# Performance work log

Hardware: AMD Instinct MI355X
Metric: run time of the kernel (lower is better)

The kernel has to match this reference:

```python
import jax, jax.numpy as jnp
import numpy as np

EPS = 1e-8  # RMSNormMultiHead default eps (forward passes self.eps)


def rms_norm_multihead(x, weight):
    # x: (B, L, H, d); normalize over last dim in float32, then scale per (H, d)
    x32 = x.astype(jnp.float32)
    normed = x32 * jax.lax.rsqrt(jnp.mean(x32 * x32, axis=-1, keepdims=True) + EPS)
    return normed.astype(x.dtype) * weight


def setup_inputs() -> dict:
    key = jax.random.key(0)
    k0, k1, k2 = jax.random.split(key, 3)
    B, L, D, H = 2, 1024, 1024, 16
    d = D // H
    X = jax.random.normal(k0, (B, L, D), dtype=jnp.float32)
    Wq = jax.random.normal(k1, (D, D), dtype=jnp.float32) * 0.02  # q_proj weight (out, in)
    Wv = jax.random.normal(k2, (D, D), dtype=jnp.float32) * 0.02  # v_proj weight (out, in)
    q_norm_w = jnp.ones((H, d), dtype=jnp.float32)
    v_norm_w = jnp.ones((H, d), dtype=jnp.float32)
    return {"X": X, "Wq": Wq, "Wv": Wv, "q_norm_w": q_norm_w, "v_norm_w": v_norm_w}


def reference(X, Wq, Wv, q_norm_w, v_norm_w):
    B, L, D = X.shape
    H, d = q_norm_w.shape
    K = X.reshape(B, L, H, d)
    Q = rms_norm_multihead((X @ Wq.T).reshape(B, L, H, d), q_norm_w)
    V = rms_norm_multihead((X @ Wv.T).reshape(B, L, H, d), v_norm_w)
    # cumulative outer-product KV state: (B, L, H, d, e)
    W = jnp.cumsum(jnp.einsum('blhd,blhe->blhde', K, V), axis=1)
    out = jnp.einsum('blhd,blhde->blhe', Q, W).reshape(B, L, D)
    return out
```

## Files before the change

### kernel.cpp

```cpp
#include <hip/hip_runtime.h>

#define BB 2
#define LL 1024
#define DD 1024
#define HH 16
#define NC 16
#define EPSF 1e-8f

typedef __attribute__((ext_vector_type(8))) short bf16x8;
typedef __attribute__((ext_vector_type(4))) float f32x4;
typedef unsigned short u16;

static __device__ inline u16 f2bf(float f) {
    unsigned int u = __builtin_bit_cast(unsigned int, f);
    u += 0x7fff + ((u >> 16) & 1);
    return (u16)(u >> 16);
}

static __device__ inline void gload_lds16(const u16* g, u16* l) {
    __builtin_amdgcn_global_load_lds((const __attribute__((address_space(1))) void*)g,
                                     (__attribute__((address_space(3))) void*)l, 16, 0, 0);
}

__global__ __launch_bounds__(256) void cvt_k(const float* __restrict__ X,
                                             const float* __restrict__ Wq,
                                             const float* __restrict__ Wv,
                                             u16* __restrict__ Xb,
                                             u16* __restrict__ Wqb,
                                             u16* __restrict__ Wvb)
{
    int i = (blockIdx.x * 256 + threadIdx.x) * 4;
    const float* s; u16* d; int off;
    if (i < 2*1024*1024)      { s = X;  d = Xb;  off = i; }
    else if (i < 3*1024*1024) { s = Wq; d = Wqb; off = i - 2*1024*1024; }
    else                      { s = Wv; d = Wvb; off = i - 3*1024*1024; }
    float4 v = *(const float4*)(s + off);
    ushort4 o;
    o.x = f2bf(v.x); o.y = f2bf(v.y); o.z = f2bf(v.z); o.w = f2bf(v.w);
    *(ushort4*)(d + off) = o;
}

__global__ __launch_bounds__(256) void gemm_fused(const u16* __restrict__ Xb,
                                                  const u16* __restrict__ Wqb,
                                                  const u16* __restrict__ Wvb,
                                                  const float* __restrict__ qw,
                                                  const float* __restrict__ vw,
                                                  u16* __restrict__ Qb,
                                                  u16* __restrict__ Vb)
{
    const int K = DD, N = DD;
    const u16* W = blockIdx.z ? Wvb : Wqb;
    const float* nw = blockIdx.z ? vw : qw;
    u16* Y = blockIdx.z ? Vb : Qb;
    __shared__ u16 As[128 * 32];
    __shared__ u16 Bs[64 * 32];

    const int tid = threadIdx.x, w = tid >> 6, lane = tid & 63;
    const int quad = lane >> 4, l16 = lane & 15;
    const int m0 = blockIdx.y * 128, n0 = blockIdx.x * 64;
    const int lrow = lane >> 2, lcol = (lane & 3) * 8;

    const u16* gA0 = Xb + (size_t)(m0 + w*16 + lrow) * K + lcol;
    const u16* gA1 = gA0 + (size_t)64 * K;
    const u16* gB0 = W + (size_t)(n0 + w*16 + lrow) * K + lcol;
    u16* lA0 = &As[(w*16) * 32];
    u16* lA1 = &As[(64 + w*16) * 32];
    u16* lB0 = &Bs[(w*16) * 32];

    f32x4 acc[2][4] = {};
    for (int k0 = 0; k0 < K; k0 += 32) {
        gload_lds16(gA0 + k0, lA0);
        gload_lds16(gA1 + k0, lA1);
        gload_lds16(gB0 + k0, lB0);
        __syncthreads();
        bf16x8 af[2], bfr[4];
        #pragma unroll
        for (int i = 0; i < 2; ++i)
            af[i] = *(const bf16x8*)&As[(w*32 + i*16 + l16) * 32 + quad*8];
        #pragma unroll
        for (int j = 0; j < 4; ++j)
            bfr[j] = *(const bf16x8*)&Bs[(j*16 + l16) * 32 + quad*8];
        #pragma unroll
        for (int i = 0; i < 2; ++i)
            #pragma unroll
            for (int j = 0; j < 4; ++j)
                acc[i][j] = __builtin_amdgcn_mfma_f32_16x16x32_bf16(af[i], bfr[j], acc[i][j], 0, 0, 0);
        __syncthreads();
    }

    float wv[4];
    #pragma unroll
    for (int j = 0; j < 4; ++j) wv[j] = nw[n0 + j*16 + l16];
    #pragma unroll
    for (int i = 0; i < 2; ++i) {
        float ss[4];
        #pragma unroll
        for (int r = 0; r < 4; ++r) {
            float s = 0.f;
            #pragma unroll
            for (int j = 0; j < 4; ++j) s += acc[i][j][r] * acc[i][j][r];
            ss[r] = s;
        }
        #pragma unroll
        for (int off = 1; off < 16; off <<= 1)
            #pragma unroll
            for (int r = 0; r < 4; ++r) ss[r] += __shfl_xor(ss[r], off, 64);
        float sc[4];
        #pragma unroll
        for (int r = 0; r < 4; ++r) sc[r] = rsqrtf(ss[r] * (1.f/64.f) + EPSF);
        #pragma unroll
        for (int r = 0; r < 4; ++r) {
            u16* yp = Y + (size_t)(m0 + w*32 + i*16 + quad*4 + r) * N + n0;
            #pragma unroll
            for (int j = 0; j < 4; ++j)
                yp[j*16 + l16] = f2bf(acc[i][j][r] * sc[r] * wv[j]);
        }
    }
}

__global__ __launch_bounds__(256) void kv_scan(const u16* __restrict__ Xb,
                                               const u16* __restrict__ Vb,
                                               u16* __restrict__ S)
{
    const int t = blockIdx.x & 3, bh = blockIdx.x >> 2;
    const int et = t & 1, dt = t >> 1;
    const int h = bh & 15, b = bh >> 4;
    __shared__ u16 Kt[32][72];
    __shared__ u16 Vt[32][72];
    const int tid = threadIdx.x, w = tid >> 6, lane = tid & 63;
    const int quad = lane >> 4, l16 = lane & 15;
    const int esub = (w & 1) * 16, dsub = (w >> 1) * 16;
    const int row = tid >> 2, q = tid & 3;

    const u16* gK = Xb + (size_t)(b*LL + row) * DD + h*64 + dt*32 + q*8;
    const u16* gV = Vb + (size_t)(b*LL + row) * DD + h*64 + et*32 + q*8;

    ushort4 kr[2], vr[2];
    kr[0] = *(const ushort4*)(gK);     kr[1] = *(const ushort4*)(gK + 4);
    vr[0] = *(const ushort4*)(gV);     vr[1] = *(const ushort4*)(gV + 4);

    f32x4 acc = {};
    for (int c = 0; c < NC; ++c) {
        #pragma unroll
        for (int i = 0; i < 4; ++i) {
            Kt[q*8 + i][row]     = ((const u16*)&kr[0])[i];
            Kt[q*8 + 4 + i][row] = ((const u16*)&kr[1])[i];
            Vt[q*8 + i][row]     = ((const u16*)&vr[0])[i];
            Vt[q*8 + 4 + i][row] = ((const u16*)&vr[1])[i];
        }
        __syncthreads();
        if (c + 1 < NC) {
            const u16* nK = gK + (size_t)(c+1)*64*DD;
            const u16* nV = gV + (size_t)(c+1)*64*DD;
            kr[0] = *(const ushort4*)(nK); kr[1] = *(const ushort4*)(nK + 4);
            vr[0] = *(const ushort4*)(nV); vr[1] = *(const ushort4*)(nV + 4);
        }
        u16* Sp = S + ((size_t)bh * NC + c) * 4096;
        #pragma unroll
        for (int r = 0; r < 4; ++r)
            Sp[(et*32 + esub + quad*4 + r) * 64 + dt*32 + dsub + l16] = f2bf(acc[r]);
        #pragma unroll
        for (int k0 = 0; k0 < 64; k0 += 32) {
            bf16x8 av = *(const bf16x8*)&Vt[esub + l16][k0 + quad*8];
            bf16x8 bv = *(const bf16x8*)&Kt[dsub + l16][k0 + quad*8];
            acc = __builtin_amdgcn_mfma_f32_16x16x32_bf16(av, bv, acc, 0, 0, 0);
        }
        __syncthreads();
    }
}

__global__ __launch_bounds__(256) void out_k(const u16* __restrict__ Xb,
                                             const u16* __restrict__ Qb,
                                             const u16* __restrict__ Vb,
                                             const u16* __restrict__ S,
                                             float* __restrict__ out)
{
    const int c = blockIdx.x & 15, bh = blockIdx.x >> 4;
    const int h = bh & 15, b = bh >> 4;
    __shared__ u16 Qs[64][72];
    __shared__ u16 Ks[64][72];
    __shared__ u16 Vt[64][72];
    __shared__ u16 St[64][72];
    const int tid = threadIdx.x;
    {
        const int row = tid >> 2, q = tid & 3;
        size_t gbase = (size_t)(b*LL + c*64 + row) * DD + h*64 + q*16;
        u16 vv[16];
        #pragma unroll
        for (int i = 0; i < 16; i += 4) {
            *(ushort4*)&Qs[row][q*16 + i] = *(const ushort4*)(Qb + gbase + i);
            *(ushort4*)&Ks[row][q*16 + i] = *(const ushort4*)(Xb + gbase + i);
            *(ushort4*)&vv[i] = *(const ushort4*)(Vb + gbase + i);
        }
        #pragma unroll
        for (int i = 0; i < 16; ++i)
            Vt[q*16 + i][row] = vv[i];
        const u16* sp = S + ((size_t)bh * NC + c) * 4096 + row*64 + q*16;
        #pragma unroll
        for (int i = 0; i < 16; i += 4)
            *(ushort4*)&St[row][q*16 + i] = *(const ushort4*)(sp + i);
    }
    __syncthreads();
    const int w = tid >> 6, lane = tid & 63, quad = lane >> 4, l16 = lane & 15;
    const int mo = (w & 1) * 32, no = (w >> 1) * 32;

    f32x4 pacc[2][2] = {};
    #pragma unroll
    for (int k0 = 0; k0 < 64; k0 += 32) {
        bf16x8 aq[2], bk[2];
        #pragma unroll
        for (int i = 0; i < 2; ++i)
            aq[i] = *(const bf16x8*)&Qs[mo + i*16 + l16][k0 + quad*8];
        #pragma unroll
        for (int j = 0; j < 2; ++j)
            bk[j] = *(const bf16x8*)&Ks[no + j*16 + l16][k0 + quad*8];
        #pragma unroll
        for (int i = 0; i < 2; ++i)
            #pragma unroll
            for (int j = 0; j < 2; ++j)
                pacc[i][j] = __builtin_amdgcn_mfma_f32_16x16x32_bf16(aq[i], bk[j], pacc[i][j], 0, 0, 0);
    }
    __syncthreads();
    #pragma unroll
    for (int i = 0; i < 2; ++i)
        #pragma unroll
        for (int j = 0; j < 2; ++j)
            #pragma unroll
            for (int r = 0; r < 4; ++r) {
                int l  = mo + i*16 + quad*4 + r;
                int lp = no + j*16 + l16;
                Ks[l][lp] = (lp <= l) ? f2bf(pacc[i][j][r]) : (u16)0;
            }
    __syncthreads();

    f32x4 acc[2][2] = {};
    #pragma unroll
    for (int k0 = 0; k0 < 64; k0 += 32) {
        bf16x8 a1[2], b1[2], a2[2], b2[2];
        #pragma unroll
        for (int i = 0; i < 2; ++i) {
            a1[i] = *(const bf16x8*)&Ks[mo + i*16 + l16][k0 + quad*8];
            a2[i] = *(const bf16x8*)&Qs[mo + i*16 + l16][k0 + quad*8];
        }
        #pragma unroll
        for (int j = 0; j < 2; ++j) {
            b1[j] = *(const bf16x8*)&Vt[no + j*16 + l16][k0 + quad*8];
            b2[j] = *(const bf16x8*)&St[no + j*16 + l16][k0 + quad*8];
        }
        #pragma unroll
        for (int i = 0; i < 2; ++i)
            #pragma unroll
            for (int j = 0; j < 2; ++j) {
                acc[i][j] = __builtin_amdgcn_mfma_f32_16x16x32_bf16(a1[i], b1[j], acc[i][j], 0, 0, 0);
                acc[i][j] = __builtin_amdgcn_mfma_f32_16x16x32_bf16(a2[i], b2[j], acc[i][j], 0, 0, 0);
            }
    }
    float* op = out + (size_t)(b*LL + c*64) * DD + h*64;
    #pragma unroll
    for (int i = 0; i < 2; ++i)
        #pragma unroll
        for (int j = 0; j < 2; ++j)
            #pragma unroll
            for (int r = 0; r < 4; ++r)
                op[(size_t)(mo + i*16 + quad*4 + r) * DD + no + j*16 + l16] = acc[i][j][r];
}

extern "C" void kernel_launch(void* const* d_in, const int* in_sizes, int n_in,
                              void* d_out, int out_size, void* d_ws, size_t ws_size,
                              hipStream_t stream) {
    const float* X  = (const float*)d_in[0];
    const float* Wq = (const float*)d_in[1];
    const float* Wv = (const float*)d_in[2];
    const float* qw = (const float*)d_in[3];
    const float* vw = (const float*)d_in[4];
    float* out = (float*)d_out;

    u16* Xb  = (u16*)d_ws;
    u16* Wqb = Xb  + (size_t)2*1024*1024;
    u16* Wvb = Wqb + (size_t)1024*1024;
    u16* Qb  = Wvb + (size_t)1024*1024;
    u16* Vb  = Qb  + (size_t)2*1024*1024;
    u16* S   = Vb  + (size_t)2*1024*1024;

    cvt_k<<<4096, 256, 0, stream>>>(X, Wq, Wv, Xb, Wqb, Wvb);
    gemm_fused<<<dim3(16, 16, 2), 256, 0, stream>>>(Xb, Wqb, Wvb, qw, vw, Qb, Vb);
    kv_scan<<<128, 256, 0, stream>>>(Xb, Vb, S);
    out_k<<<BB*HH*NC, 256, 0, stream>>>(Xb, Qb, Vb, S, out);
}
```

Measured before the change: 110.4 us.

## Double-buffer kv_scan, widen GEMM k-step, and coalesce state layout

The projection GEMM now loads two 32-wide K slices per iteration into separate LDS buffers, which halves the number of barrier pairs in the K loop. kv_scan double-buffers its transposed K/V tiles and splits the loading so half the threads fetch K and half fetch V, prefetching two chunks ahead. It also stores the chunk state in MFMA fragment order so writes are contiguous. out_k is updated to decode that permuted layout when filling its LDS tile. The cost is more LDS and registers per block, and a more intricate index mapping between the two kernels.

```diff
diff --git a/kernel.cpp b/kernel.cpp
--- a/kernel.cpp
+++ b/kernel.cpp
@@ -52,8 +52,8 @@
     const u16* W = blockIdx.z ? Wvb : Wqb;
     const float* nw = blockIdx.z ? vw : qw;
     u16* Y = blockIdx.z ? Vb : Qb;
-    __shared__ u16 As[128 * 32];
-    __shared__ u16 Bs[64 * 32];
+    __shared__ u16 As0[128 * 32], As1[128 * 32];
+    __shared__ u16 Bs0[64 * 32],  Bs1[64 * 32];
 
     const int tid = threadIdx.x, w = tid >> 6, lane = tid & 63;
     const int quad = lane >> 4, l16 = lane & 15;
@@ -63,28 +63,36 @@
     const u16* gA0 = Xb + (size_t)(m0 + w*16 + lrow) * K + lcol;
     const u16* gA1 = gA0 + (size_t)64 * K;
     const u16* gB0 = W + (size_t)(n0 + w*16 + lrow) * K + lcol;
-    u16* lA0 = &As[(w*16) * 32];
-    u16* lA1 = &As[(64 + w*16) * 32];
-    u16* lB0 = &Bs[(w*16) * 32];
+    u16* lA0_0 = &As0[(w*16) * 32];      u16* lA0_1 = &As1[(w*16) * 32];
+    u16* lA1_0 = &As0[(64 + w*16) * 32]; u16* lA1_1 = &As1[(64 + w*16) * 32];
+    u16* lB0_0 = &Bs0[(w*16) * 32];      u16* lB0_1 = &Bs1[(w*16) * 32];
 
     f32x4 acc[2][4] = {};
-    for (int k0 = 0; k0 < K; k0 += 32) {
-        gload_lds16(gA0 + k0, lA0);
-        gload_lds16(gA1 + k0, lA1);
-        gload_lds16(gB0 + k0, lB0);
+    for (int k0 = 0; k0 < K; k0 += 64) {
+        gload_lds16(gA0 + k0,      lA0_0);
+        gload_lds16(gA0 + k0 + 32, lA0_1);
+        gload_lds16(gA1 + k0,      lA1_0);
+        gload_lds16(gA1 + k0 + 32, lA1_1);
+        gload_lds16(gB0 + k0,      lB0_0);
+        gload_lds16(gB0 + k0 + 32, lB0_1);
         __syncthreads();
-        bf16x8 af[2], bfr[4];
-        #pragma unroll
-        for (int i = 0; i < 2; ++i)
-            af[i] = *(const bf16x8*)&As[(w*32 + i*16 + l16) * 32 + quad*8];
-        #pragma unroll
-        for (int j = 0; j < 4; ++j)
-            bfr[j] = *(const bf16x8*)&Bs[(j*16 + l16) * 32 + quad*8];
-        #pragma unroll
-        for (int i = 0; i < 2; ++i)
+        #pragma unroll
+        for (int hh = 0; hh < 2; ++hh) {
+            const u16* Ah = hh ? As1 : As0;
+            const u16* Bh = hh ? Bs1 : Bs0;
+            bf16x8 af[2], bfr[4];
+            #pragma unroll
+            for (int i = 0; i < 2; ++i)
+                af[i] = *(const bf16x8*)&Ah[(w*32 + i*16 + l16) * 32 + quad*8];
             #pragma unroll
             for (int j = 0; j < 4; ++j)
-                acc[i][j] = __builtin_amdgcn_mfma_f32_16x16x32_bf16(af[i], bfr[j], acc[i][j], 0, 0, 0);
+                bfr[j] = *(const bf16x8*)&Bh[(j*16 + l16) * 32 + quad*8];
+            #pragma unroll
+            for (int i = 0; i < 2; ++i)
+                #pragma unroll
+                for (int j = 0; j < 4; ++j)
+                    acc[i][j] = __builtin_amdgcn_mfma_f32_16x16x32_bf16(af[i], bfr[j], acc[i][j], 0, 0, 0);
+        }
         __syncthreads();
     }
 
@@ -125,44 +133,42 @@
     const int t = blockIdx.x & 3, bh = blockIdx.x >> 2;
     const int et = t & 1, dt = t >> 1;
     const int h = bh & 15, b = bh >> 4;
-    __shared__ u16 Kt[32][72];
-    __shared__ u16 Vt[32][72];
+    __shared__ u16 Kt[2][32][72];
+    __shared__ u16 Vt[2][32][72];
     const int tid = threadIdx.x, w = tid >> 6, lane = tid & 63;
     const int quad = lane >> 4, l16 = lane & 15;
     const int esub = (w & 1) * 16, dsub = (w >> 1) * 16;
-    const int row = tid >> 2, q = tid & 3;
-
-    const u16* gK = Xb + (size_t)(b*LL + row) * DD + h*64 + dt*32 + q*8;
-    const u16* gV = Vb + (size_t)(b*LL + row) * DD + h*64 + et*32 + q*8;
-
-    ushort4 kr[2], vr[2];
-    kr[0] = *(const ushort4*)(gK);     kr[1] = *(const ushort4*)(gK + 4);
-    vr[0] = *(const ushort4*)(gV);     vr[1] = *(const ushort4*)(gV + 4);
-
+    const int half = tid >> 7, hrow = (tid & 127) >> 1, hq = tid & 1;
+    const u16* gsrc = (half ? Vb : Xb) + (size_t)(b*LL + hrow) * DD
+                      + h*64 + (half ? et : dt) * 32 + hq*16;
+    u16 (*Tb)[32][72] = half ? Vt : Kt;
+    ushort4 rr[4];
+
+    auto loadc = [&](int c) {
+        const u16* p = gsrc + (size_t)c * 64 * DD;
+        rr[0] = *(const ushort4*)(p);      rr[1] = *(const ushort4*)(p + 4);
+        rr[2] = *(const ushort4*)(p + 8);  rr[3] = *(const ushort4*)(p + 12);
+    };
+    auto writec = [&](int buf) {
+        #pragma unroll
+        for (int i = 0; i < 16; ++i)
+            Tb[buf][hq*16 + i][hrow] = ((const u16*)rr)[i];
+    };
+
+    loadc(0); writec(0); loadc(1);
+    __syncthreads();
     f32x4 acc = {};
     for (int c = 0; c < NC; ++c) {
-        #pragma unroll
-        for (int i = 0; i < 4; ++i) {
-            Kt[q*8 + i][row]     = ((const u16*)&kr[0])[i];
-            Kt[q*8 + 4 + i][row] = ((const u16*)&kr[1])[i];
-            Vt[q*8 + i][row]     = ((const u16*)&vr[0])[i];
-            Vt[q*8 + 4 + i][row] = ((const u16*)&vr[1])[i];
-        }
-        __syncthreads();
-        if (c + 1 < NC) {
-            const u16* nK = gK + (size_t)(c+1)*64*DD;
-            const u16* nV = gV + (size_t)(c+1)*64*DD;
-            kr[0] = *(const ushort4*)(nK); kr[1] = *(const ushort4*)(nK + 4);
-            vr[0] = *(const ushort4*)(nV); vr[1] = *(const ushort4*)(nV + 4);
-        }
-        u16* Sp = S + ((size_t)bh * NC + c) * 4096;
-        #pragma unroll
-        for (int r = 0; r < 4; ++r)
-            Sp[(et*32 + esub + quad*4 + r) * 64 + dt*32 + dsub + l16] = f2bf(acc[r]);
+        const int cur = c & 1;
+        if (c + 1 < NC) writec(1 - cur);
+        if (c + 2 < NC) loadc(c + 2);
+        u16* Sp = S + (((size_t)(bh*NC + c)) << 12) + t*1024 + w*256;
+        #pragma unroll
+        for (int r = 0; r < 4; ++r) Sp[r*64 + lane] = f2bf(acc[r]);
         #pragma unroll
         for (int k0 = 0; k0 < 64; k0 += 32) {
-            bf16x8 av = *(const bf16x8*)&Vt[esub + l16][k0 + quad*8];
-            bf16x8 bv = *(const bf16x8*)&Kt[dsub + l16][k0 + quad*8];
+            bf16x8 av = *(const bf16x8*)&Vt[cur][esub + l16][k0 + quad*8];
+            bf16x8 bv = *(const bf16x8*)&Kt[cur][dsub + l16][k0 + quad*8];
             acc = __builtin_amdgcn_mfma_f32_16x16x32_bf16(av, bv, acc, 0, 0, 0);
         }
         __syncthreads();
@@ -195,10 +201,16 @@
         #pragma unroll
         for (int i = 0; i < 16; ++i)
             Vt[q*16 + i][row] = vv[i];
-        const u16* sp = S + ((size_t)bh * NC + c) * 4096 + row*64 + q*16;
-        #pragma unroll
-        for (int i = 0; i < 16; i += 4)
-            *(ushort4*)&St[row][q*16 + i] = *(const ushort4*)(sp + i);
+        const u16* Sc = S + (((size_t)(bh*NC + c)) << 12);
+        #pragma unroll
+        for (int j = 0; j < 4; ++j) {
+            int f = (tid + j*256) * 4;
+            ushort4 sv = *(const ushort4*)(Sc + f);
+            int tt = f >> 10, ww = (f >> 8) & 3, rr_ = (f >> 6) & 3, ln = f & 63;
+            int e = (tt & 1)*32 + (ww & 1)*16 + (ln >> 4)*4 + rr_;
+            int d = (tt >> 1)*32 + ((ww >> 1) & 1)*16 + (ln & 15);
+            *(ushort4*)&St[e][d] = sv;
+        }
     }
     __syncthreads();
     const int w = tid >> 6, lane = tid & 63, quad = lane >> 4, l16 = lane & 15;
```

New measurement: 106.2 us. 3.8% less time.
